# Optimization experiments

Measured on AMD Instinct MI355X. Metric: run time of the kernel, lower is better.

## Reference

```python
import jax, jax.numpy as jnp
import numpy as np

E, NH, NL, NP = 256, 8, 3, 4
HD = E // NH  # 32
SPATIAL = np.array([[100, 100], [50, 50], [25, 25]], dtype=np.int64)  # (H_l, W_l)


def setup_inputs() -> dict:
    key = jax.random.key(0)
    ks = jax.random.split(key, 12)
    Lv = int(SPATIAL.prod(1).sum())  # 13125
    B, Lq = 4, Lv
    query = jax.random.normal(ks[0], (B, Lq, E), jnp.float32)
    value = jax.random.normal(ks[1], (B, Lv, E), jnp.float32)
    reference_points = jax.random.uniform(ks[2], (B, Lq, NL, 2), dtype=jnp.float32)
    s = 1.0 / np.sqrt(E)
    Wv = jax.random.normal(ks[3], (E, E), jnp.float32) * s
    bv = jnp.zeros((E,), jnp.float32)
    Wo = jax.random.normal(ks[4], (E, E), jnp.float32) * s
    bo = jnp.zeros((E,), jnp.float32)
    # sampling_offsets: small random weight, grid-init bias (as in _reset_parameters)
    Woff = jax.random.normal(ks[5], (E, NH * NL * NP * 2), jnp.float32) * 0.01
    thetas = np.arange(NH, dtype=np.float32) * (2.0 * np.pi / NH)
    grid = np.stack([np.cos(thetas), np.sin(thetas)], -1)
    grid = grid / np.abs(grid).max(-1, keepdims=True)
    grid = np.tile(grid[:, None, None, :], (1, NL, NP, 1)) * np.arange(1, NP + 1, dtype=np.float32)[None, None, :, None]
    boff = jnp.asarray(grid.reshape(-1), jnp.float32)
    Watt = jax.random.normal(ks[6], (E, NH * NL * NP), jnp.float32) * 0.01
    batt = jnp.zeros((NH * NL * NP,), jnp.float32)
    return {
        "query": query, "reference_points": reference_points, "value": value,
        "value_spatial_shapes": jnp.asarray(SPATIAL),
        "Wv": Wv, "bv": bv, "Woff": Woff, "boff": boff,
        "Watt": Watt, "batt": batt, "Wo": Wo, "bo": bo,
    }


def _bilinear_sample(vl, x, y, Hl, Wl):
    """vl: (B, NH, Hl*Wl, HD); x, y: (B, Lq, NH, NP) pixel coords (align_corners=False).
    Returns (B, Lq, NH, NP, HD) with zero padding outside, matching F.grid_sample."""
    B, Lq = x.shape[0], x.shape[1]
    x0 = jnp.floor(x)
    y0 = jnp.floor(y)
    x0i = x0.astype(jnp.int32)
    y0i = y0.astype(jnp.int32)
    wx1 = x - x0
    wy1 = y - y0
    acc = jnp.zeros((B, Lq, NH, NP, HD), vl.dtype)
    for yi, wy in ((y0i, 1.0 - wy1), (y0i + 1, wy1)):
        for xi, wx in ((x0i, 1.0 - wx1), (x0i + 1, wx1)):
            valid = (xi >= 0) & (xi < Wl) & (yi >= 0) & (yi < Hl)
            idx = jnp.clip(yi, 0, Hl - 1) * Wl + jnp.clip(xi, 0, Wl - 1)  # (B,Lq,NH,NP)
            idxf = idx.transpose(0, 2, 1, 3).reshape(B, NH, Lq * NP)
            g = jnp.take_along_axis(vl, idxf[..., None], axis=2)  # (B,NH,Lq*NP,HD)
            g = g.reshape(B, NH, Lq, NP, HD).transpose(0, 2, 1, 3, 4)
            w = (wx * wy) * valid.astype(vl.dtype)
            acc = acc + g * w[..., None]
    return acc


def reference(query, reference_points, value, value_spatial_shapes,
              Wv, bv, Woff, boff, Watt, batt, Wo, bo):
    shapes = np.asarray(jax.device_get(value_spatial_shapes))  # static level metadata
    B, Lq, _ = query.shape
    v = value @ Wv + bv  # (B, Lv, E)
    v = v.reshape(B, -1, NH, HD)
    off = (query @ Woff + boff).reshape(B, Lq, NH, NL, NP, 2)
    aw = (query @ Watt + batt).reshape(B, Lq, NH, NL * NP)
    aw = jax.nn.softmax(aw, axis=-1).reshape(B, Lq, NH, NL, NP)
    # normalizer is (W_l, H_l)
    norm = jnp.asarray(np.stack([shapes[:, 1], shapes[:, 0]], -1), jnp.float32)  # (NL, 2)
    locs = reference_points[:, :, None, :, None, :] + off / norm[None, None, None, :, None, :]
    splits = np.cumsum(shapes.prod(1))[:-1].tolist()
    v_levels = jnp.split(v, splits, axis=1)
    out = jnp.zeros((B, Lq, NH, HD), v.dtype)
    for l in range(NL):
        Hl, Wl = int(shapes[l, 0]), int(shapes[l, 1])
        vl = v_levels[l].transpose(0, 2, 1, 3)  # (B, NH, Hl*Wl, HD)
        # grid_sample(align_corners=False): pixel = loc * size - 0.5
        x = locs[:, :, :, l, :, 0] * Wl - 0.5
        y = locs[:, :, :, l, :, 1] * Hl - 0.5
        samp = _bilinear_sample(vl, x, y, Hl, Wl)  # (B,Lq,NH,NP,HD)
        out = out + jnp.einsum('bqhpd,bqhp->bqhd', samp, aw[:, :, :, l, :])
    out = out.reshape(B, Lq, E)
    return out @ Wo + bo
```

## Files before the change

kernel.cpp:

```cpp
#include <hip/hip_runtime.h>
#include <hip/hip_bf16.h>
#include <hip/hip_fp16.h>

#define E    256
#define NH   8
#define NL   3
#define NP   4
#define HD   32
#define LQ   13125

typedef short bf16x8 __attribute__((ext_vector_type(8)));
typedef _Float16 f16x8 __attribute__((ext_vector_type(8)));
typedef float f32x4  __attribute__((ext_vector_type(4)));

__device__ __forceinline__ ushort f2bf(float x) {
  uint u = __float_as_uint(x);
  uint r = (u + 0x7fffu + ((u >> 16) & 1u)) >> 16;
  return (ushort)r;
}
__device__ __forceinline__ float bf2f(ushort u) {
  return __uint_as_float((uint)u << 16);
}
__device__ __forceinline__ ushort f2h(float x) {
  return __half_as_ushort(__float2half(x));
}
__device__ __forceinline__ __half2 u2h2(uint u) {
  union { uint u; __half2 h; } c; c.u = u; return c.h;
}
__device__ __forceinline__ uint h22u(__half2 h) {
  union { uint u; __half2 h; } c; c.h = h; return c.u;
}

__device__ __forceinline__ void gl_lds16(const ushort* g, ushort* l) {
  __builtin_amdgcn_global_load_lds(
      (const __attribute__((address_space(1))) void*)g,
      (__attribute__((address_space(3))) void*)l, 16, 0, 0);
}

__device__ __forceinline__ bf16x8 cvt8(const float* p) {
  const float4 a = *(const float4*)p;
  const float4 b = *(const float4*)(p + 4);
  bf16x8 r;
  r[0] = (short)f2bf(a.x); r[1] = (short)f2bf(a.y);
  r[2] = (short)f2bf(a.z); r[3] = (short)f2bf(a.w);
  r[4] = (short)f2bf(b.x); r[5] = (short)f2bf(b.y);
  r[6] = (short)f2bf(b.z); r[7] = (short)f2bf(b.w);
  return r;
}

__global__ __launch_bounds__(512) void gemm_wide_v(
    const float* __restrict__ A32, const ushort* __restrict__ B_,
    const float* __restrict__ bias, ushort* __restrict__ Cf16, int M) {
  __shared__ ushort As[4096];
  __shared__ ushort Bs[8192];
  const int tid = threadIdx.x;
  const int lane = tid & 63;
  const int wid = tid >> 6;
  const int wm = wid >> 2, wn = wid & 3;
  const int r0 = blockIdx.x * 128;
  const int l15 = lane & 15;
  const int lhi = lane >> 4;

  f32x4 acc[4][4] = {};

  for (int kk = 0; kk < 256; kk += 32) {
    {
      const int arow = min(r0 + (tid >> 2), M - 1);
      *(bf16x8*)&As[tid * 8] =
          cvt8(A32 + (size_t)arow * 256 + kk + (tid & 3) * 8);
    }
#pragma unroll
    for (int rr = 0; rr < 2; ++rr) {
      const int u = rr * 512 + tid;
      const int brow = u >> 2;
      gl_lds16(B_ + (size_t)brow * 256 + kk + (u & 3) * 8,
               Bs + rr * 4096 + wid * 512);
    }
    __syncthreads();

    bf16x8 af[4], bf[4];
#pragma unroll
    for (int mi = 0; mi < 4; ++mi)
      af[mi] = *(const bf16x8*)&As[(wm * 64 + mi * 16 + l15) * 32 + lhi * 8];
#pragma unroll
    for (int ni = 0; ni < 4; ++ni)
      bf[ni] = *(const bf16x8*)&Bs[(wn * 64 + ni * 16 + l15) * 32 + lhi * 8];
#pragma unroll
    for (int mi = 0; mi < 4; ++mi)
#pragma unroll
      for (int ni = 0; ni < 4; ++ni)
        acc[mi][ni] = __builtin_amdgcn_mfma_f32_16x16x32_bf16(
            af[mi], bf[ni], acc[mi][ni], 0, 0, 0);
    __syncthreads();
  }

#pragma unroll
  for (int ni = 0; ni < 4; ++ni) {
    const int col = wn * 64 + ni * 16 + l15;
    const float bb = bias[col];
    const int h = col >> 5, d = col & 31;
#pragma unroll
    for (int mi = 0; mi < 4; ++mi) {
      const int rowb = r0 + wm * 64 + mi * 16 + lhi * 4;
#pragma unroll
      for (int r = 0; r < 4; ++r) {
        const int row = rowb + r;
        if (row >= M) continue;
        const int bidx = row / LQ, pos = row - bidx * LQ;
        Cf16[((size_t)(bidx * NH + h) * LQ + pos) * HD + d] =
            f2h(acc[mi][ni][r] + bb);
      }
    }
  }
}

__global__ __launch_bounds__(512) void gemm_q_pack(
    const float* __restrict__ A32, const ushort* __restrict__ B_,
    const float* __restrict__ bias, const float* __restrict__ ref,
    uint* __restrict__ samp, int M) {
  __shared__ __align__(16) char ldsbuf[37 * 1024];
  ushort* As = (ushort*)ldsbuf;
  ushort* Bs = (ushort*)(ldsbuf + 8192);
  float* panel = (float*)ldsbuf;

  const int tid = threadIdx.x;
  const int lane = tid & 63;
  const int wid = tid >> 6;
  const int rg = wid >> 1;
  const int cg = wid & 1;
  const int r0 = blockIdx.x * 128;
  const int l15 = lane & 15;
  const int lhi = lane >> 4;

  f32x4 acc[2][9] = {};

  for (int kk = 0; kk < 256; kk += 32) {
    {
      const int arow = min(r0 + (tid >> 2), M - 1);
      *(bf16x8*)&As[tid * 8] =
          cvt8(A32 + (size_t)arow * 256 + kk + (tid & 3) * 8);
    }
#pragma unroll
    for (int rr = 0; rr < 3; ++rr) {
      const int u = rr * 512 + tid;
      if (u < 1152)
        gl_lds16(B_ + (size_t)(u >> 2) * 256 + kk + (u & 3) * 8,
                 Bs + (u >> 2) * 32 + (u & 3) * 8);
    }
    __syncthreads();

    bf16x8 af[2], bf[9];
#pragma unroll
    for (int mi = 0; mi < 2; ++mi)
      af[mi] = *(const bf16x8*)&As[(rg * 32 + mi * 16 + l15) * 32 + lhi * 8];
#pragma unroll
    for (int ni = 0; ni < 9; ++ni)
      bf[ni] = *(const bf16x8*)&Bs[(cg * 144 + ni * 16 + l15) * 32 + lhi * 8];
#pragma unroll
    for (int mi = 0; mi < 2; ++mi)
#pragma unroll
      for (int ni = 0; ni < 9; ++ni)
        acc[mi][ni] = __builtin_amdgcn_mfma_f32_16x16x32_bf16(
            af[mi], bf[ni], acc[mi][ni], 0, 0, 0);
    __syncthreads();
  }

  const float S_[3] = {100.f, 50.f, 25.f};
  const int Wl_[3] = {100, 50, 25};
#pragma unroll
  for (int c = 0; c < 4; ++c) {
    if (rg == c) {
#pragma unroll
      for (int mi = 0; mi < 2; ++mi)
#pragma unroll
        for (int ni = 0; ni < 9; ++ni) {
          const int col = cg * 144 + ni * 16 + l15;
          const float bb = bias[col];
          const int rl = mi * 16 + lhi * 4;
#pragma unroll
          for (int r = 0; r < 4; ++r)
            panel[(rl + r) * 289 + col] = acc[mi][ni][r] + bb;
        }
    }
    __syncthreads();
    if (tid < 256) {
      const int r = tid >> 3, h = tid & 7;
      const int g = r0 + c * 32 + r;
      if (g < M) {
        const float* rg_ = &panel[r * 289];
        float xy[24], lg[12];
#pragma unroll
        for (int j = 0; j < 24; ++j) xy[j] = rg_[h * 24 + j];
#pragma unroll
        for (int j = 0; j < 12; ++j) lg[j] = rg_[192 + h * 12 + j];
        float rx[3], ry[3];
#pragma unroll
        for (int l = 0; l < 3; ++l) {
          rx[l] = ref[(size_t)g * 6 + l * 2 + 0];
          ry[l] = ref[(size_t)g * 6 + l * 2 + 1];
        }
        float m = lg[0];
#pragma unroll
        for (int j = 1; j < 12; ++j) m = fmaxf(m, lg[j]);
        float e[12], s = 0.f;
#pragma unroll
        for (int j = 0; j < 12; ++j) { e[j] = __expf(lg[j] - m); s += e[j]; }
        const float inv = 1.f / s;

        uint out[36];
#pragma unroll
        for (int l = 0; l < 3; ++l) {
          const int Wl = Wl_[l];
#pragma unroll
          for (int p = 0; p < 4; ++p) {
            const int j = l * 4 + p;
            const float x = rx[l] * S_[l] + xy[l * 8 + p * 2 + 0] - 0.5f;
            const float y = ry[l] * S_[l] + xy[l * 8 + p * 2 + 1] - 0.5f;
            const float w = e[j] * inv;
            const float fx = floorf(x), fy = floorf(y);
            const int x0 = (int)fx, y0 = (int)fy;
            const float wx1 = x - fx, wy1 = y - fy;
            const float wx0 = 1.f - wx1, wy0 = 1.f - wy1;
            const int x0c = min(max(x0, 0), Wl - 1);
            const int x1c = min(max(x0 + 1, 0), Wl - 1);
            const int y0c = min(max(y0, 0), Wl - 1);
            const int y1c = min(max(y0 + 1, 0), Wl - 1);
            const float vx0 = (x0 >= 0 && x0 < Wl) ? wx0 : 0.f;
            const float vx1 = (x0 + 1 >= 0 && x0 + 1 < Wl) ? wx1 : 0.f;
            const float vy0 = (y0 >= 0 && y0 < Wl) ? wy0 : 0.f;
            const float vy1 = (y0 + 1 >= 0 && y0 + 1 < Wl) ? wy1 : 0.f;
            const int idx00 = y0c * Wl + x0c;
            const uint meta = (uint)(x1c - x0c) | ((uint)((y1c - y0c) * Wl) << 1);
            out[j * 3 + 0] = (uint)idx00 | (meta << 16);
            out[j * 3 + 1] = (uint)f2h(w * vy0 * vx0) | ((uint)f2h(w * vy0 * vx1) << 16);
            out[j * 3 + 2] = (uint)f2h(w * vy1 * vx0) | ((uint)f2h(w * vy1 * vx1) << 16);
          }
        }
        uint4* o4 = (uint4*)(samp + (size_t)g * 288 + h * 36);
#pragma unroll
        for (int i = 0; i < 9; ++i)
          o4[i] = make_uint4(out[i * 4 + 0], out[i * 4 + 1],
                             out[i * 4 + 2], out[i * 4 + 3]);
      }
    }
    __syncthreads();
  }
}

__global__ __launch_bounds__(512) void gemm_wide_o(
    const ushort* __restrict__ A16, const ushort* __restrict__ B_,
    const float* __restrict__ bias, float* __restrict__ C, int M) {
  __shared__ ushort As[4096];
  __shared__ ushort Bs[8192];
  const int tid = threadIdx.x;
  const int lane = tid & 63;
  const int wid = tid >> 6;
  const int wm = wid >> 2, wn = wid & 3;
  const int r0 = blockIdx.x * 128;
  const int l15 = lane & 15;
  const int lhi = lane >> 4;

  f32x4 acc[4][4] = {};

  for (int kk = 0; kk < 256; kk += 32) {
    {
      const int arow = min(r0 + wid * 16 + (lane >> 2), M - 1);
      gl_lds16(A16 + (size_t)arow * 256 + kk + (lane & 3) * 8,
               As + wid * 512);
    }
#pragma unroll
    for (int rr = 0; rr < 2; ++rr) {
      const int u = rr * 512 + tid;
      const int brow = u >> 2;
      gl_lds16(B_ + (size_t)brow * 256 + kk + (u & 3) * 8,
               Bs + rr * 4096 + wid * 512);
    }
    __syncthreads();

    f16x8 af[4], bf[4];
#pragma unroll
    for (int mi = 0; mi < 4; ++mi)
      af[mi] = *(const f16x8*)&As[(wm * 64 + mi * 16 + l15) * 32 + lhi * 8];
#pragma unroll
    for (int ni = 0; ni < 4; ++ni)
      bf[ni] = *(const f16x8*)&Bs[(wn * 64 + ni * 16 + l15) * 32 + lhi * 8];
#pragma unroll
    for (int mi = 0; mi < 4; ++mi)
#pragma unroll
      for (int ni = 0; ni < 4; ++ni)
        acc[mi][ni] = __builtin_amdgcn_mfma_f32_16x16x32_f16(
            af[mi], bf[ni], acc[mi][ni], 0, 0, 0);
    __syncthreads();
  }

#pragma unroll
  for (int ni = 0; ni < 4; ++ni) {
    const int col = wn * 64 + ni * 16 + l15;
    const float bb = bias[col];
#pragma unroll
    for (int mi = 0; mi < 4; ++mi) {
      const int rowb = r0 + wm * 64 + mi * 16 + lhi * 4;
#pragma unroll
      for (int r = 0; r < 4; ++r) {
        const int row = rowb + r;
        if (row < M) C[(size_t)row * 256 + col] = acc[mi][ni][r] + bb;
      }
    }
  }
}

__global__ __launch_bounds__(256) void convert_W(
    const float* __restrict__ Wv, const float* __restrict__ Woff,
    const float* __restrict__ Watt, const float* __restrict__ Wo,
    const float* __restrict__ boff, const float* __restrict__ batt,
    ushort* __restrict__ WvT, ushort* __restrict__ WcT,
    ushort* __restrict__ WoT, float* __restrict__ bias288) {
  const int t = blockIdx.x * 256 + threadIdx.x;
  if (t < 256 * 256) {
    const int n = t >> 8, k = t & 255;
    WvT[t] = f2bf(Wv[k * 256 + n]);
    WoT[t] = f2h(Wo[k * 256 + n]);
  }
  if (t < 288 * 256) {
    const int n = t >> 8, k = t & 255;
    const float w = (n < 192) ? Woff[k * 192 + n] : Watt[k * 96 + (n - 192)];
    WcT[t] = f2bf(w);
  }
  if (t < 288) bias288[t] = (t < 192) ? boff[t] : batt[t - 192];
}

template <int SQ>
__device__ __forceinline__ void deform_body(
    const uint* __restrict__ sd, const char* __restrict__ vb, int xs,
    __half2& A0, __half2& A1, __half2& A2, __half2& A3) {
  const int loff_[3] = {0, 10000, 12500};
#pragma unroll
  for (int t = 0; t < 6; ++t) {
    const int j = 2 * t + SQ;
    const uint d0 = sd[j * 3 + 0];
    const int idx00 = (int)(d0 & 0xffffu);
    const uint meta = d0 >> 16;
    const int dx = (int)(meta & 1u);
    const int dyW = (int)(meta >> 1);
    const uint d1 = sd[j * 3 + 1];
    const uint d2 = sd[j * 3 + 2];
    const uint w0_ = xs ? (d1 >> 16) : (d1 & 0xffffu);
    const uint w1_ = xs ? (d2 >> 16) : (d2 & 0xffffu);
    const uint offA = (uint)(loff_[j >> 2] + idx00 + (xs ? dx : 0)) * (HD * 2);
    const uint offB = offA + (uint)dyW * (HD * 2);
    const uint4 c0 = *(const uint4*)(vb + offA);
    const uint4 c1 = *(const uint4*)(vb + offB);
    const __half2 w0 = u2h2(w0_ | (w0_ << 16));
    const __half2 w1 = u2h2(w1_ | (w1_ << 16));
    A0 = __hfma2(w0, u2h2(c0.x), A0);
    A1 = __hfma2(w0, u2h2(c0.y), A1);
    A2 = __hfma2(w0, u2h2(c0.z), A2);
    A3 = __hfma2(w0, u2h2(c0.w), A3);
    A0 = __hfma2(w1, u2h2(c1.x), A0);
    A1 = __hfma2(w1, u2h2(c1.y), A1);
    A2 = __hfma2(w1, u2h2(c1.z), A2);
    A3 = __hfma2(w1, u2h2(c1.w), A3);
  }
}

__global__ __launch_bounds__(256) void deform_packed(
    const ushort* __restrict__ vbf, const uint* __restrict__ samp,
    ushort* __restrict__ mid, int nq) {
  const int tid = threadIdx.x;
  const int pair = blockIdx.x & 31;
  const int qc = blockIdx.x >> 5;
  const int q = qc * 16 + (tid >> 4);
  if (q >= nq) return;
  const int lane16 = tid & 15;
  const int sq = lane16 >> 3;
  const int xs = (lane16 >> 2) & 1;
  const int cq = lane16 & 3;
  const int h = pair & 7;
  const int b = pair >> 3;
  const int g = b * nq + q;

  const uint4* sp = (const uint4*)(samp + (size_t)g * 288 + h * 36);
  const char* vb = (const char*)(vbf + ((size_t)pair * nq) * HD + cq * 8);

  uint4 s[9];
#pragma unroll
  for (int i = 0; i < 9; ++i) s[i] = sp[i];
  uint sd[36];
#pragma unroll
  for (int i = 0; i < 9; ++i) {
    sd[4 * i + 0] = s[i].x; sd[4 * i + 1] = s[i].y;
    sd[4 * i + 2] = s[i].z; sd[4 * i + 3] = s[i].w;
  }

  __half2 A0 = __float2half2_rn(0.f), A1 = A0, A2 = A0, A3 = A0;
  if (sq == 0) deform_body<0>(sd, vb, xs, A0, A1, A2, A3);
  else         deform_body<1>(sd, vb, xs, A0, A1, A2, A3);

  A0 = __hadd2(A0, u2h2(__shfl_xor(h22u(A0), 8)));
  A1 = __hadd2(A1, u2h2(__shfl_xor(h22u(A1), 8)));
  A2 = __hadd2(A2, u2h2(__shfl_xor(h22u(A2), 8)));
  A3 = __hadd2(A3, u2h2(__shfl_xor(h22u(A3), 8)));
  A0 = __hadd2(A0, u2h2(__shfl_xor(h22u(A0), 4)));
  A1 = __hadd2(A1, u2h2(__shfl_xor(h22u(A1), 4)));
  A2 = __hadd2(A2, u2h2(__shfl_xor(h22u(A2), 4)));
  A3 = __hadd2(A3, u2h2(__shfl_xor(h22u(A3), 4)));

  if ((lane16 >> 2) == 0) {
    uint4 o;
    o.x = h22u(A0); o.y = h22u(A1); o.z = h22u(A2); o.w = h22u(A3);
    *(uint4*)&mid[(size_t)g * E + h * HD + cq * 8] = o;
  }
}

extern "C" void kernel_launch(void* const* d_in, const int* in_sizes, int n_in,
                              void* d_out, int out_size, void* d_ws, size_t ws_size,
                              hipStream_t stream) {
  const float* query = (const float*)d_in[0];
  const float* refpt = (const float*)d_in[1];
  const float* value = (const float*)d_in[2];
  const float* Wv   = (const float*)d_in[4];
  const float* bv   = (const float*)d_in[5];
  const float* Woff = (const float*)d_in[6];
  const float* boff = (const float*)d_in[7];
  const float* Watt = (const float*)d_in[8];
  const float* batt = (const float*)d_in[9];
  const float* Wo   = (const float*)d_in[10];
  const float* bo   = (const float*)d_in[11];

  const int M = in_sizes[0] / E;
  const int nq = LQ;
  const int nb = M / nq;

  float* wsf   = (float*)d_ws;
  float* raw   = wsf;
  float* b288  = raw + (size_t)M * 288;
  ushort* mid  = (ushort*)(b288 + 288);
  ushort* vbf  = mid + (size_t)M * 256;
  ushort* wvT  = vbf + (size_t)M * 256;
  ushort* woT  = wvT + 65536;
  ushort* wcT  = woT + 65536;

  const int gridM = (M + 127) / 128;

  convert_W<<<288, 256, 0, stream>>>(Wv, Woff, Watt, Wo, boff, batt,
                                     wvT, wcT, woT, b288);
  gemm_wide_v<<<gridM, 512, 0, stream>>>(value, wvT, bv, vbf, M);
  gemm_q_pack<<<gridM, 512, 0, stream>>>(
      query, wcT, b288, refpt, (uint*)raw, M);
  const int qchunks = (nq + 15) / 16;
  deform_packed<<<qchunks * 32, 256, 0, stream>>>(
      vbf, (const uint*)raw, mid, nq);
  gemm_wide_o<<<gridM, 512, 0, stream>>>(mid, woT, bo, (float*)d_out, M);
}
```

Before: 183.4 us.

## Precompute byte offsets in sample records and stage records via shared memory

The packing kernel now stores the full byte offset of each sample's top-left texel, including the level offset, plus x/y step flags in the upper bits. The deform kernel decodes these offsets more cheaply and loads the per-query records cooperatively into shared memory with coalesced loads. It now uses 8 lanes per query instead of 16, so each thread walks all 12 samples and the first cross-lane reduction step is dropped. This trades some parallelism per query for less redundant record loading and less index arithmetic, and it packs offsets into 20 bits, which relies on the value buffer offsets fitting in that range.

```diff
diff --git a/kernel.cpp b/kernel.cpp
--- a/kernel.cpp
+++ b/kernel.cpp
@@ -167,6 +167,7 @@
 
   const float S_[3] = {100.f, 50.f, 25.f};
   const int Wl_[3] = {100, 50, 25};
+  const int loff_[3] = {0, 10000, 12500};
 #pragma unroll
   for (int c = 0; c < 4; ++c) {
     if (rg == c) {
@@ -229,9 +230,9 @@
             const float vx1 = (x0 + 1 >= 0 && x0 + 1 < Wl) ? wx1 : 0.f;
             const float vy0 = (y0 >= 0 && y0 < Wl) ? wy0 : 0.f;
             const float vy1 = (y0 + 1 >= 0 && y0 + 1 < Wl) ? wy1 : 0.f;
-            const int idx00 = y0c * Wl + x0c;
-            const uint meta = (uint)(x1c - x0c) | ((uint)((y1c - y0c) * Wl) << 1);
-            out[j * 3 + 0] = (uint)idx00 | (meta << 16);
+            const uint base = (uint)(loff_[l] + y0c * Wl + x0c) * 64u;
+            out[j * 3 + 0] = base | ((uint)(x1c - x0c) << 20)
+                                  | ((uint)(y1c != y0c) << 21);
             out[j * 3 + 1] = (uint)f2h(w * vy0 * vx0) | ((uint)f2h(w * vy0 * vx1) << 16);
             out[j * 3 + 2] = (uint)f2h(w * vy1 * vx0) | ((uint)f2h(w * vy1 * vx1) << 16);
           }
@@ -329,27 +330,60 @@
   if (t < 288) bias288[t] = (t < 192) ? boff[t] : batt[t - 192];
 }
 
-template <int SQ>
-__device__ __forceinline__ void deform_body(
-    const uint* __restrict__ sd, const char* __restrict__ vb, int xs,
-    __half2& A0, __half2& A1, __half2& A2, __half2& A3) {
-  const int loff_[3] = {0, 10000, 12500};
-#pragma unroll
-  for (int t = 0; t < 6; ++t) {
-    const int j = 2 * t + SQ;
+__global__ __launch_bounds__(256) void deform_packed(
+    const ushort* __restrict__ vbf, const uint* __restrict__ samp,
+    ushort* __restrict__ mid, int nq) {
+  __shared__ __align__(16) uint recs[32][36];
+  const int tid = threadIdx.x;
+  const int pair = blockIdx.x & 31;
+  const int qc = blockIdx.x >> 5;
+  const int h = pair & 7;
+  const int b = pair >> 3;
+  const int q0 = qc * 32;
+
+  for (int i = tid; i < 288; i += 256) {
+    const int qi = i / 9, di = (i - qi * 9) * 4;
+    const int q = q0 + qi;
+    if (q < nq)
+      *(uint4*)&recs[qi][di] =
+          *(const uint4*)&samp[((size_t)(b * nq + q)) * 288 + h * 36 + di];
+  }
+  __syncthreads();
+
+  const int qi = tid >> 3;
+  const int q = q0 + qi;
+  if (q >= nq) return;
+  const int lane8 = tid & 7;
+  const int xs = lane8 >> 2;
+  const int cq = lane8 & 3;
+  const int g = b * nq + q;
+
+  const char* vb = (const char*)(vbf + ((size_t)pair * nq) * HD + cq * 8);
+
+  uint4 r4[9];
+#pragma unroll
+  for (int i = 0; i < 9; ++i) r4[i] = *(const uint4*)&recs[qi][i * 4];
+  uint sd[36];
+#pragma unroll
+  for (int i = 0; i < 9; ++i) {
+    sd[4 * i + 0] = r4[i].x; sd[4 * i + 1] = r4[i].y;
+    sd[4 * i + 2] = r4[i].z; sd[4 * i + 3] = r4[i].w;
+  }
+
+  const uint LB_[3] = {6400u, 3200u, 1600u};
+  __half2 A0 = __float2half2_rn(0.f), A1 = A0, A2 = A0, A3 = A0;
+#pragma unroll
+  for (int j = 0; j < 12; ++j) {
     const uint d0 = sd[j * 3 + 0];
-    const int idx00 = (int)(d0 & 0xffffu);
-    const uint meta = d0 >> 16;
-    const int dx = (int)(meta & 1u);
-    const int dyW = (int)(meta >> 1);
     const uint d1 = sd[j * 3 + 1];
     const uint d2 = sd[j * 3 + 2];
+    const uint base = d0 & 0xFFFFFu;
+    const uint offA = base + (xs ? ((d0 >> 14) & 64u) : 0u);
+    const uint offB = offA + ((d0 & (1u << 21)) ? LB_[j >> 2] : 0u);
+    const uint4 c0 = *(const uint4*)(vb + offA);
+    const uint4 c1 = *(const uint4*)(vb + offB);
     const uint w0_ = xs ? (d1 >> 16) : (d1 & 0xffffu);
     const uint w1_ = xs ? (d2 >> 16) : (d2 & 0xffffu);
-    const uint offA = (uint)(loff_[j >> 2] + idx00 + (xs ? dx : 0)) * (HD * 2);
-    const uint offB = offA + (uint)dyW * (HD * 2);
-    const uint4 c0 = *(const uint4*)(vb + offA);
-    const uint4 c1 = *(const uint4*)(vb + offB);
     const __half2 w0 = u2h2(w0_ | (w0_ << 16));
     const __half2 w1 = u2h2(w1_ | (w1_ << 16));
     A0 = __hfma2(w0, u2h2(c0.x), A0);
@@ -361,51 +395,13 @@
     A2 = __hfma2(w1, u2h2(c1.z), A2);
     A3 = __hfma2(w1, u2h2(c1.w), A3);
   }
-}
-
-__global__ __launch_bounds__(256) void deform_packed(
-    const ushort* __restrict__ vbf, const uint* __restrict__ samp,
-    ushort* __restrict__ mid, int nq) {
-  const int tid = threadIdx.x;
-  const int pair = blockIdx.x & 31;
-  const int qc = blockIdx.x >> 5;
-  const int q = qc * 16 + (tid >> 4);
-  if (q >= nq) return;
-  const int lane16 = tid & 15;
-  const int sq = lane16 >> 3;
-  const int xs = (lane16 >> 2) & 1;
-  const int cq = lane16 & 3;
-  const int h = pair & 7;
-  const int b = pair >> 3;
-  const int g = b * nq + q;
-
-  const uint4* sp = (const uint4*)(samp + (size_t)g * 288 + h * 36);
-  const char* vb = (const char*)(vbf + ((size_t)pair * nq) * HD + cq * 8);
-
-  uint4 s[9];
-#pragma unroll
-  for (int i = 0; i < 9; ++i) s[i] = sp[i];
-  uint sd[36];
-#pragma unroll
-  for (int i = 0; i < 9; ++i) {
-    sd[4 * i + 0] = s[i].x; sd[4 * i + 1] = s[i].y;
-    sd[4 * i + 2] = s[i].z; sd[4 * i + 3] = s[i].w;
-  }
-
-  __half2 A0 = __float2half2_rn(0.f), A1 = A0, A2 = A0, A3 = A0;
-  if (sq == 0) deform_body<0>(sd, vb, xs, A0, A1, A2, A3);
-  else         deform_body<1>(sd, vb, xs, A0, A1, A2, A3);
-
-  A0 = __hadd2(A0, u2h2(__shfl_xor(h22u(A0), 8)));
-  A1 = __hadd2(A1, u2h2(__shfl_xor(h22u(A1), 8)));
-  A2 = __hadd2(A2, u2h2(__shfl_xor(h22u(A2), 8)));
-  A3 = __hadd2(A3, u2h2(__shfl_xor(h22u(A3), 8)));
+
   A0 = __hadd2(A0, u2h2(__shfl_xor(h22u(A0), 4)));
   A1 = __hadd2(A1, u2h2(__shfl_xor(h22u(A1), 4)));
   A2 = __hadd2(A2, u2h2(__shfl_xor(h22u(A2), 4)));
   A3 = __hadd2(A3, u2h2(__shfl_xor(h22u(A3), 4)));
 
-  if ((lane16 >> 2) == 0) {
+  if (xs == 0) {
     uint4 o;
     o.x = h22u(A0); o.y = h22u(A1); o.z = h22u(A2); o.w = h22u(A3);
     *(uint4*)&mid[(size_t)g * E + h * HD + cq * 8] = o;
@@ -447,7 +443,7 @@
   gemm_wide_v<<<gridM, 512, 0, stream>>>(value, wvT, bv, vbf, M);
   gemm_q_pack<<<gridM, 512, 0, stream>>>(
       query, wcT, b288, refpt, (uint*)raw, M);
-  const int qchunks = (nq + 15) / 16;
+  const int qchunks = (nq + 31) / 32;
   deform_packed<<<qchunks * 32, 256, 0, stream>>>(
       vbf, (const uint*)raw, mid, nq);
   gemm_wide_o<<<gridM, 512, 0, stream>>>(mid, woT, bo, (float*)d_out, M);
```

Measured after the change: 180.4 us. Within noise of the previous version (-1.6%).
